# Kernel tuning notes

Measured on AMD Instinct MI355X. Metric: run time of the kernel, lower is better.

Reference implementation:

```python
import jax, jax.numpy as jnp
import numpy as np

H = 16
D_MODEL = 1024
D_K = D_MODEL // H


def setup_inputs() -> dict:
    key = jax.random.key(0)
    ks = jax.random.split(key, 11)
    B, S, D = 2, 2048, D_MODEL
    sc = 1.0 / np.sqrt(D)
    return {
        "query": jax.random.normal(ks[0], (B, S, D), jnp.float32),
        "key": jax.random.normal(ks[1], (B, S, D), jnp.float32),
        "value": jax.random.normal(ks[2], (B, S, D), jnp.float32),
        "Wq": jax.random.normal(ks[3], (D, D), jnp.float32) * sc,
        "bq": jnp.zeros((D,), jnp.float32),
        "Wk": jax.random.normal(ks[4], (D, D), jnp.float32) * sc,
        "bk": jnp.zeros((D,), jnp.float32),
        "Wv": jax.random.normal(ks[5], (D, D), jnp.float32) * sc,
        "bv": jnp.zeros((D,), jnp.float32),
        "Wo": jax.random.normal(ks[6], (D, D), jnp.float32) * sc,
        "bo": jnp.zeros((D,), jnp.float32),
    }


def _split_heads(x, B, S):
    # [B,S,D] -> [B,H,S,d_k]
    return x.reshape(B, S, H, D_K).transpose(0, 2, 1, 3)


def reference(query, key, value, Wq, bq, Wk, bk, Wv, bv, Wo, bo):
    B, S, D = query.shape
    q = _split_heads(query @ Wq + bq, B, S)
    k = _split_heads(key @ Wk + bk, B, key.shape[1])
    v = _split_heads(value @ Wv + bv, B, value.shape[1])
    scores = jnp.einsum("bhqd,bhkd->bhqk", q, k) / jnp.sqrt(jnp.asarray(D_K, q.dtype))
    p_attn = jax.nn.softmax(scores, axis=-1)  # dropout is identity at inference
    x = jnp.einsum("bhqk,bhkd->bhqd", p_attn, v)
    x = x.transpose(0, 2, 1, 3).reshape(B, S, H * D_K)
    return x @ Wo + bo
```

## Files before the change

### kernel.cpp

```cpp
#include <hip/hip_runtime.h>

typedef unsigned short u16;
typedef unsigned int   u32;
typedef __bf16 bf16x8 __attribute__((ext_vector_type(8)));
typedef float  f32x4  __attribute__((ext_vector_type(4)));

__device__ __forceinline__ u16 f2bf(float f) {
  u32 u = __float_as_uint(f);
  u += 0x7fffu + ((u >> 16) & 1u);
  return (u16)(u >> 16);
}

__device__ __forceinline__ u32 cvt_pk_bf16(float a, float b) {
  u32 r;
  asm("v_cvt_pk_bf16_f32 %0, %1, %2" : "=v"(r) : "v"(a), "v"(b));
  return r;
}

__device__ __forceinline__ float max3f(float a, float b, float c) {
  float r;
  asm("v_max3_f32 %0, %1, %2, %3" : "=v"(r) : "v"(a), "v"(b), "v"(c));
  return r;
}

__device__ __forceinline__ void gll16(const void* g, void* l) {
  __builtin_amdgcn_global_load_lds(
      (__attribute__((address_space(1))) unsigned int*)(g),
      (__attribute__((address_space(3))) unsigned int*)(l), 16, 0, 0);
}

__device__ __forceinline__ int xcd_swz(int wg, int nwg) {
  int cpx = nwg >> 3;
  return (wg & 7) * cpx + (wg >> 3);
}

__device__ __forceinline__ void cvt8(const float* __restrict__ s, u16* __restrict__ d, int o) {
  float4 a = *(const float4*)(s + o);
  float4 b = *(const float4*)(s + o + 4);
  uint4 r;
  r.x = cvt_pk_bf16(a.x, a.y);
  r.y = cvt_pk_bf16(a.z, a.w);
  r.z = cvt_pk_bf16(b.x, b.y);
  r.w = cvt_pk_bf16(b.z, b.w);
  *(uint4*)(d + o) = r;
}

__global__ __launch_bounds__(256) void convert_in(
    const float* __restrict__ q, const float* __restrict__ k, const float* __restrict__ v,
    u16* __restrict__ qo, u16* __restrict__ ko, u16* __restrict__ vo) {
  int t = blockIdx.x * 256 + threadIdx.x;
  int o = t * 8;
  cvt8(q, qo, o);
  cvt8(k, ko, o);
  cvt8(v, vo, o);
}

__global__ __launch_bounds__(256) void convert_w(
    const float* __restrict__ Wq, const float* __restrict__ Wk,
    const float* __restrict__ Wv, const float* __restrict__ Wo,
    u16* __restrict__ Wqt, u16* __restrict__ Wkt,
    u16* __restrict__ Wvt, u16* __restrict__ Wot) {
  __shared__ __align__(16) u16 t[64][72];
  int z = blockIdx.z;
  const float* W = (z == 0) ? Wq : (z == 1) ? Wk : (z == 2) ? Wv : Wo;
  u16* Wt = (z == 0) ? Wqt : (z == 1) ? Wkt : (z == 2) ? Wvt : Wot;
  int k0 = blockIdx.y * 64, n0 = blockIdx.x * 64;
  int tid = threadIdx.x;
#pragma unroll
  for (int e = 0; e < 4; ++e) {
    int i = e * 256 + tid;
    int r = i >> 4, c4 = (i & 15) * 4;
    float4 vv = *(const float4*)(W + (size_t)(k0 + r) * 1024 + n0 + c4);
    union { u16 u[4]; uint2 w2; } p;
    p.u[0] = f2bf(vv.x); p.u[1] = f2bf(vv.y); p.u[2] = f2bf(vv.z); p.u[3] = f2bf(vv.w);
    *(uint2*)&t[r][c4] = p.w2;
  }
  __syncthreads();
#pragma unroll
  for (int e = 0; e < 2; ++e) {
    int i = e * 256 + tid;
    int rn = i >> 3, c8 = (i & 7) * 8;
    union { u16 u[8]; uint4 w4; } p;
#pragma unroll
    for (int kk = 0; kk < 8; ++kk) p.u[kk] = t[c8 + kk][rn];
    *(uint4*)(Wt + (size_t)(n0 + rn) * 1024 + k0 + c8) = p.w4;
  }
}

__device__ __forceinline__ void gemm_core(
    const u16* __restrict__ A,
    const u16* __restrict__ Bt,
    int K, int m0, int n0,
    u16* As, u16* Bs, f32x4 acc[4][4]) {
  const int tid = threadIdx.x;
  const int l = tid & 63;
  const int g = l >> 4, q16 = l & 15;
  const int wv = tid >> 6;
  const int wr = wv >> 1, wc = wv & 1;
#pragma unroll
  for (int mi = 0; mi < 4; ++mi)
#pragma unroll
    for (int ni = 0; ni < 4; ++ni) acc[mi][ni] = (f32x4){0.f, 0.f, 0.f, 0.f};

  for (int k0 = 0; k0 < K; k0 += 64) {
    __syncthreads();
#pragma unroll
    for (int c = 0; c < 4; ++c) {
      int i = c * 256 + tid;
      int row = i >> 3, ce = (i & 7) * 8;
      gll16(A + (size_t)(m0 + row) * K + k0 + ce, As + i * 8);
      gll16(Bt + (size_t)(n0 + row) * K + k0 + ce, Bs + i * 8);
    }
    __syncthreads();
#pragma unroll
    for (int kb = 0; kb < 2; ++kb) {
      bf16x8 af[4], bfr[4];
#pragma unroll
      for (int mi = 0; mi < 4; ++mi)
        af[mi] = *(const bf16x8*)(As + (wr * 64 + mi * 16 + q16) * 64 + kb * 32 + g * 8);
#pragma unroll
      for (int ni = 0; ni < 4; ++ni)
        bfr[ni] = *(const bf16x8*)(Bs + (wc * 64 + ni * 16 + q16) * 64 + kb * 32 + g * 8);
#pragma unroll
      for (int mi = 0; mi < 4; ++mi)
#pragma unroll
        for (int ni = 0; ni < 4; ++ni)
          acc[mi][ni] = __builtin_amdgcn_mfma_f32_16x16x32_bf16(af[mi], bfr[ni], acc[mi][ni], 0, 0, 0);
    }
  }
}

__global__ __launch_bounds__(256) void gemm_qkv(
    const u16* __restrict__ qA, const u16* __restrict__ kA, const u16* __restrict__ vA,
    const u16* __restrict__ qW, const u16* __restrict__ kW, const u16* __restrict__ vW,
    const float* __restrict__ qb, const float* __restrict__ kb2, const float* __restrict__ vb,
    u16* __restrict__ Qh, u16* __restrict__ Kh, u16* __restrict__ Vh, float qscale) {
  __shared__ __align__(16) u16 As[128 * 64];
  __shared__ __align__(16) u16 Bs[128 * 64];
  int z = blockIdx.z;
  const u16* A   = (z == 0) ? qA : (z == 1) ? kA : vA;
  const u16* Bt  = (z == 0) ? qW : (z == 1) ? kW : vW;
  const float* bias = (z == 0) ? qb : (z == 1) ? kb2 : vb;
  u16* out = (z == 0) ? Qh : (z == 1) ? Kh : Vh;
  float scale = (z == 0) ? qscale : 1.0f;
  int swz = xcd_swz(blockIdx.y * gridDim.x + blockIdx.x, gridDim.x * gridDim.y);
  int m0 = (swz >> 3) * 128, n0 = (swz & 7) * 128;
  f32x4 acc[4][4];
  gemm_core(A, Bt, 1024, m0, n0, As, Bs, acc);

  const int tid = threadIdx.x;
  const int l = tid & 63;
  const int g = l >> 4, q16 = l & 15;
  const int wv = tid >> 6;
  const int wr = wv >> 1, wc = wv & 1;
#pragma unroll
  for (int ni = 0; ni < 4; ++ni) {
    int n = n0 + wc * 64 + ni * 16 + q16;
    float bvv = bias[n];
    int hh = n >> 6, dk = n & 63;
#pragma unroll
    for (int mi = 0; mi < 4; ++mi) {
#pragma unroll
      for (int j = 0; j < 4; ++j) {
        int m = m0 + wr * 64 + mi * 16 + g * 4 + j;
        int b = m >> 11, s = m & 2047;
        float v = (acc[mi][ni][j] + bvv) * scale;
        out[(((size_t)b * 16 + hh) * 2048 + s) * 64 + dk] = f2bf(v);
      }
    }
  }
}

__global__ __launch_bounds__(256) void gemm_out(
    const u16* __restrict__ A, const u16* __restrict__ Bt,
    const float* __restrict__ bias, float* __restrict__ Out) {
  __shared__ __align__(16) u16 As[128 * 64];
  __shared__ __align__(16) u16 Bs[128 * 64];
  int swz = xcd_swz(blockIdx.y * gridDim.x + blockIdx.x, gridDim.x * gridDim.y);
  int m0 = (swz >> 3) * 128, n0 = (swz & 7) * 128;
  f32x4 acc[4][4];
  gemm_core(A, Bt, 1024, m0, n0, As, Bs, acc);

  const int tid = threadIdx.x;
  const int l = tid & 63;
  const int g = l >> 4, q16 = l & 15;
  const int wv = tid >> 6;
  const int wr = wv >> 1, wc = wv & 1;
#pragma unroll
  for (int ni = 0; ni < 4; ++ni) {
    int n = n0 + wc * 64 + ni * 16 + q16;
    float bvv = bias[n];
#pragma unroll
    for (int mi = 0; mi < 4; ++mi) {
#pragma unroll
      for (int j = 0; j < 4; ++j) {
        int m = m0 + wr * 64 + mi * 16 + g * 4 + j;
        Out[(size_t)m * 1024 + n] = acc[mi][ni][j] + bvv;
      }
    }
  }
}

__global__ __launch_bounds__(256) void transpose_v(const u16* __restrict__ Vh, u16* __restrict__ Vt) {
  __shared__ __align__(16) u16 t[64][72];
  int bh = blockIdx.y, s0 = blockIdx.x * 64;
  int tid = threadIdx.x;
#pragma unroll
  for (int e = 0; e < 2; ++e) {
    int i = e * 256 + tid;
    int r = i >> 3, c8 = (i & 7) * 8;
    uint4 vv = *(const uint4*)(Vh + ((size_t)bh * 2048 + s0 + r) * 64 + c8);
    *(uint4*)&t[r][c8] = vv;
  }
  __syncthreads();
#pragma unroll
  for (int e = 0; e < 2; ++e) {
    int i = e * 256 + tid;
    int d = i >> 3, s8 = (i & 7) * 8;
    union { u16 u[8]; uint4 w4; } p;
#pragma unroll
    for (int kk = 0; kk < 8; ++kk) p.u[kk] = t[s8 + kk][d];
    *(uint4*)(Vt + ((size_t)bh * 64 + d) * 2048 + s0 + s8) = p.w4;
  }
}

__global__ __launch_bounds__(512) void attn_kernel(
    const u16* __restrict__ Qh,
    const u16* __restrict__ Kh,
    const u16* __restrict__ Vt,
    u16* __restrict__ Xb) {
  __shared__ __align__(16) u16 Ks[3][64 * 64];
  __shared__ __align__(16) u16 Vs[3][64 * 64];
  __shared__ __align__(16) u16 Ps[8][16][72];

  const int tid = threadIdx.x;
  const int l = tid & 63, wv = tid >> 6;
  const int g = l >> 4, q16 = l & 15;
  const int swz = xcd_swz(blockIdx.y * gridDim.x + blockIdx.x, gridDim.x * gridDim.y);
  const int qblk = swz & 15, bh = swz >> 4;
  const int b = bh >> 4, h = bh & 15;
  const int qrow0 = qblk * 128 + wv * 16;

  const int srow = tid >> 3;
  const int sc8  = (tid & 7) ^ (srow & 7);
  const u16* Kbase = Kh + (size_t)bh * 2048 * 64;
  const u16* Vbase = Vt + (size_t)bh * 64 * 2048;

  bf16x8 bq[2];
#pragma unroll
  for (int kb = 0; kb < 2; ++kb)
    bq[kb] = *(const bf16x8*)(Qh + ((size_t)bh * 2048 + qrow0 + q16) * 64 + kb * 32 + g * 8);

  f32x4 x[4];
#pragma unroll
  for (int ni = 0; ni < 4; ++ni) x[ni] = (f32x4){0.f, 0.f, 0.f, 0.f};
  float m_run = -3e38f, l_run = 0.f;

  gll16(Kbase + (size_t)srow * 64 + sc8 * 8, &Ks[0][tid * 8]);
  gll16(Vbase + (size_t)srow * 2048 + sc8 * 8, &Vs[0][tid * 8]);
  gll16(Kbase + ((size_t)64 + srow) * 64 + sc8 * 8, &Ks[1][tid * 8]);
  gll16(Vbase + (size_t)srow * 2048 + 64 + sc8 * 8, &Vs[1][tid * 8]);
  asm volatile("s_waitcnt vmcnt(2)" ::: "memory");
  __builtin_amdgcn_s_barrier();

  for (int kt = 0; kt < 32; ++kt) {
    const int cb = kt % 3;
    if (kt + 2 < 32) {
      const int pb = (kt + 2) % 3;
      gll16(Kbase + ((size_t)(kt + 2) * 64 + srow) * 64 + sc8 * 8, &Ks[pb][tid * 8]);
      gll16(Vbase + (size_t)srow * 2048 + (kt + 2) * 64 + sc8 * 8, &Vs[pb][tid * 8]);
    }

    f32x4 st[4];
#pragma unroll
    for (int mi = 0; mi < 4; ++mi) st[mi] = (f32x4){0.f, 0.f, 0.f, 0.f};
#pragma unroll
    for (int mi = 0; mi < 4; ++mi) {
      int row = mi * 16 + q16;
#pragma unroll
      for (int kb = 0; kb < 2; ++kb) {
        int pc8 = (kb * 4 + g) ^ (row & 7);
        bf16x8 ak = *(const bf16x8*)(&Ks[cb][row * 64 + pc8 * 8]);
        st[mi] = __builtin_amdgcn_mfma_f32_16x16x32_bf16(ak, bq[kb], st[mi], 0, 0, 0);
      }
    }

    float ma = max3f(st[0][0], st[0][1], st[0][2]);
    ma = max3f(ma, st[0][3], st[1][0]);
    ma = max3f(ma, st[1][1], st[1][2]);
    ma = fmaxf(ma, st[1][3]);
    float mb = max3f(st[2][0], st[2][1], st[2][2]);
    mb = max3f(mb, st[2][3], st[3][0]);
    mb = max3f(mb, st[3][1], st[3][2]);
    mb = fmaxf(mb, st[3][3]);
    float mx = fmaxf(ma, mb);
    mx = fmaxf(mx, __shfl_xor(mx, 16));
    mx = fmaxf(mx, __shfl_xor(mx, 32));

    float mref, sf;
    if (__all(mx <= m_run + 8.f)) {
      mref = m_run; sf = 1.f;
    } else {
      mref = fmaxf(m_run, mx);
      sf = __builtin_amdgcn_exp2f(m_run - mref);
      m_run = mref;
#pragma unroll
      for (int j = 0; j < 4; ++j) {
        float sfx = __shfl(sf, g * 4 + j);
#pragma unroll
        for (int ni = 0; ni < 4; ++ni) x[ni][j] *= sfx;
      }
    }

    float rs = 0.f;
#pragma unroll
    for (int mi = 0; mi < 4; ++mi)
#pragma unroll
      for (int j = 0; j < 4; ++j) {
        float p = __builtin_amdgcn_exp2f(st[mi][j] - mref);
        st[mi][j] = p;
        rs += p;
      }
    rs += __shfl_xor(rs, 16);
    rs += __shfl_xor(rs, 32);
    l_run = l_run * sf + rs;

#pragma unroll
    for (int mi = 0; mi < 4; ++mi) {
      uint2 w;
      w.x = cvt_pk_bf16(st[mi][0], st[mi][1]);
      w.y = cvt_pk_bf16(st[mi][2], st[mi][3]);
      *(uint2*)&Ps[wv][q16][mi * 16 + g * 4] = w;
    }

#pragma unroll
    for (int kkb = 0; kkb < 2; ++kkb) {
      bf16x8 ap = *(const bf16x8*)&Ps[wv][q16][kkb * 32 + g * 8];
#pragma unroll
      for (int ni = 0; ni < 4; ++ni) {
        int d = ni * 16 + q16;
        int pc8 = (kkb * 4 + g) ^ (d & 7);
        bf16x8 vf = *(const bf16x8*)(&Vs[cb][d * 64 + pc8 * 8]);
        x[ni] = __builtin_amdgcn_mfma_f32_16x16x32_bf16(ap, vf, x[ni], 0, 0, 0);
      }
    }

    if (kt < 30) {
      asm volatile("s_waitcnt vmcnt(2)" ::: "memory");
    } else {
      asm volatile("s_waitcnt vmcnt(0)" ::: "memory");
    }
    __builtin_amdgcn_s_barrier();
  }

  float li = 1.0f / l_run;
#pragma unroll
  for (int j = 0; j < 4; ++j) {
    float lv = __shfl(li, g * 4 + j);
    int srw = b * 2048 + qblk * 128 + wv * 16 + g * 4 + j;
#pragma unroll
    for (int ni = 0; ni < 4; ++ni) {
      int col = h * 64 + ni * 16 + q16;
      Xb[(size_t)srw * 1024 + col] = f2bf(x[ni][j] * lv);
    }
  }
}

extern "C" void kernel_launch(void* const* d_in, const int* in_sizes, int n_in,
                              void* d_out, int out_size, void* d_ws, size_t ws_size,
                              hipStream_t stream) {
  (void)in_sizes; (void)n_in; (void)out_size; (void)ws_size;
  const float* q  = (const float*)d_in[0];
  const float* k  = (const float*)d_in[1];
  const float* v  = (const float*)d_in[2];
  const float* Wq = (const float*)d_in[3];
  const float* bq = (const float*)d_in[4];
  const float* Wk = (const float*)d_in[5];
  const float* bk = (const float*)d_in[6];
  const float* Wv = (const float*)d_in[7];
  const float* bv = (const float*)d_in[8];
  const float* Wo = (const float*)d_in[9];
  const float* bo = (const float*)d_in[10];

  char* W = (char*)d_ws;
  const size_t MB = 1ull << 20;
  u16* qbf = (u16*)(W + 0 * MB);
  u16* kbf = (u16*)(W + 8 * MB);
  u16* vbf = (u16*)(W + 16 * MB);
  u16* wqt = (u16*)(W + 24 * MB);
  u16* wkt = (u16*)(W + 26 * MB);
  u16* wvt = (u16*)(W + 28 * MB);
  u16* wot = (u16*)(W + 30 * MB);
  u16* Qh  = (u16*)(W + 32 * MB);
  u16* Kh  = (u16*)(W + 40 * MB);
  u16* Vh  = (u16*)(W + 48 * MB);
  u16* Vtb = (u16*)(W + 56 * MB);
  u16* Xb  = (u16*)(W + 64 * MB);

  convert_in<<<2048, 256, 0, stream>>>(q, k, v, qbf, kbf, vbf);
  convert_w<<<dim3(16, 16, 4), 256, 0, stream>>>(Wq, Wk, Wv, Wo, wqt, wkt, wvt, wot);
  const float QSCALE = 0.125f * 1.4426950408889634f;
  gemm_qkv<<<dim3(8, 32, 3), 256, 0, stream>>>(qbf, kbf, vbf, wqt, wkt, wvt,
                                               bq, bk, bv, Qh, Kh, Vh, QSCALE);
  transpose_v<<<dim3(32, 32), 256, 0, stream>>>(Vh, Vtb);
  attn_kernel<<<dim3(16, 32), 512, 0, stream>>>(Qh, Kh, Vtb, Xb);
  gemm_out<<<dim3(8, 32), 256, 0, stream>>>(Xb, wot, bo, (float*)d_out);
}
```

Baseline: 152.2 us.

## Load V fragments directly to registers and transpose P with permlane swaps

Removes the shared-memory staging buffers for V and for the probability tile P. V fragments are now read straight from global memory into registers at the start of each key tile. The softmax output is rearranged into MFMA A-operand layout with v_permlane32/16_swap instead of an LDS write and read. A minimum-occupancy hint is added to the launch bounds. The aim is to cut LDS traffic and footprint and so allow more resident blocks, at the cost of V loads that are no longer prefetched two tiles ahead and whose latency may be exposed.

```diff
diff --git a/kernel.cpp b/kernel.cpp
--- a/kernel.cpp
+++ b/kernel.cpp
@@ -224,14 +224,12 @@
   }
 }
 
-__global__ __launch_bounds__(512) void attn_kernel(
+__global__ __launch_bounds__(512, 4) void attn_kernel(
     const u16* __restrict__ Qh,
     const u16* __restrict__ Kh,
     const u16* __restrict__ Vt,
     u16* __restrict__ Xb) {
   __shared__ __align__(16) u16 Ks[3][64 * 64];
-  __shared__ __align__(16) u16 Vs[3][64 * 64];
-  __shared__ __align__(16) u16 Ps[8][16][72];
 
   const int tid = threadIdx.x;
   const int l = tid & 63, wv = tid >> 6;
@@ -257,19 +255,23 @@
   float m_run = -3e38f, l_run = 0.f;
 
   gll16(Kbase + (size_t)srow * 64 + sc8 * 8, &Ks[0][tid * 8]);
-  gll16(Vbase + (size_t)srow * 2048 + sc8 * 8, &Vs[0][tid * 8]);
   gll16(Kbase + ((size_t)64 + srow) * 64 + sc8 * 8, &Ks[1][tid * 8]);
-  gll16(Vbase + (size_t)srow * 2048 + 64 + sc8 * 8, &Vs[1][tid * 8]);
-  asm volatile("s_waitcnt vmcnt(2)" ::: "memory");
+  asm volatile("s_waitcnt vmcnt(1)" ::: "memory");
   __builtin_amdgcn_s_barrier();
 
   for (int kt = 0; kt < 32; ++kt) {
     const int cb = kt % 3;
-    if (kt + 2 < 32) {
-      const int pb = (kt + 2) % 3;
-      gll16(Kbase + ((size_t)(kt + 2) * 64 + srow) * 64 + sc8 * 8, &Ks[pb][tid * 8]);
-      gll16(Vbase + (size_t)srow * 2048 + (kt + 2) * 64 + sc8 * 8, &Vs[pb][tid * 8]);
-    }
+
+    bf16x8 vf[2][4];
+#pragma unroll
+    for (int kkb = 0; kkb < 2; ++kkb)
+#pragma unroll
+      for (int ni = 0; ni < 4; ++ni)
+        vf[kkb][ni] = *(const bf16x8*)(Vbase + (size_t)(ni * 16 + q16) * 2048 +
+                                       kt * 64 + kkb * 32 + g * 8);
+
+    if (kt + 2 < 32)
+      gll16(Kbase + ((size_t)(kt + 2) * 64 + srow) * 64 + sc8 * 8, &Ks[(kt + 2) % 3][tid * 8]);
 
     f32x4 st[4];
 #pragma unroll
@@ -325,30 +327,32 @@
     rs += __shfl_xor(rs, 32);
     l_run = l_run * sf + rs;
 
-#pragma unroll
-    for (int mi = 0; mi < 4; ++mi) {
-      uint2 w;
-      w.x = cvt_pk_bf16(st[mi][0], st[mi][1]);
-      w.y = cvt_pk_bf16(st[mi][2], st[mi][3]);
-      *(uint2*)&Ps[wv][q16][mi * 16 + g * 4] = w;
-    }
-
+    bf16x8 ap[2];
 #pragma unroll
     for (int kkb = 0; kkb < 2; ++kkb) {
-      bf16x8 ap = *(const bf16x8*)&Ps[wv][q16][kkb * 32 + g * 8];
-#pragma unroll
-      for (int ni = 0; ni < 4; ++ni) {
-        int d = ni * 16 + q16;
-        int pc8 = (kkb * 4 + g) ^ (d & 7);
-        bf16x8 vf = *(const bf16x8*)(&Vs[cb][d * 64 + pc8 * 8]);
-        x[ni] = __builtin_amdgcn_mfma_f32_16x16x32_bf16(ap, vf, x[ni], 0, 0, 0);
-      }
-    }
-
-    if (kt < 30) {
-      asm volatile("s_waitcnt vmcnt(2)" ::: "memory");
-    } else {
+      u32 a0 = cvt_pk_bf16(st[kkb * 2][0],     st[kkb * 2][1]);
+      u32 a1 = cvt_pk_bf16(st[kkb * 2][2],     st[kkb * 2][3]);
+      u32 b0 = cvt_pk_bf16(st[kkb * 2 + 1][0], st[kkb * 2 + 1][1]);
+      u32 b1 = cvt_pk_bf16(st[kkb * 2 + 1][2], st[kkb * 2 + 1][3]);
+      asm("v_permlane32_swap_b32 %0, %1" : "+v"(a0), "+v"(b0));
+      asm("v_permlane16_swap_b32 %0, %1" : "+v"(a0), "+v"(b0));
+      asm("v_permlane32_swap_b32 %0, %1" : "+v"(a1), "+v"(b1));
+      asm("v_permlane16_swap_b32 %0, %1" : "+v"(a1), "+v"(b1));
+      union { u32 u[4]; bf16x8 v; } pk_;
+      pk_.u[0] = a0; pk_.u[1] = a1; pk_.u[2] = b0; pk_.u[3] = b1;
+      ap[kkb] = pk_.v;
+    }
+
+#pragma unroll
+    for (int kkb = 0; kkb < 2; ++kkb)
+#pragma unroll
+      for (int ni = 0; ni < 4; ++ni)
+        x[ni] = __builtin_amdgcn_mfma_f32_16x16x32_bf16(ap[kkb], vf[kkb][ni], x[ni], 0, 0, 0);
+
+    if (kt == 30) {
       asm volatile("s_waitcnt vmcnt(0)" ::: "memory");
+    } else if (kt < 30) {
+      asm volatile("s_waitcnt vmcnt(1)" ::: "memory");
     }
     __builtin_amdgcn_s_barrier();
   }
```

Result: slower. 230.7 us (+51.6%).
